# Kernel optimization log

Hardware: AMD Instinct MI355X
Metric: run time of the kernel (lower is better)

The kernel has to match this reference:

```python
import jax, jax.numpy as jnp
import numpy as np

N, CIN, C, COUT, K27, KNN_K = 65536, 1, 128, 128, 27, 16
C4, C2 = C // 4, C // 2


def _w(key, shape, fan_in):
    return (jax.random.normal(key, shape, dtype=jnp.float32) * (fan_in ** -0.5))


def setup_inputs() -> dict:
    key = jax.random.key(0)
    ks = jax.random.split(key, 32)
    inp = {
        "feats": jax.random.normal(ks[0], (N, CIN), dtype=jnp.float32),
        # kernel-map neighbor indices; value N means 'no neighbor at this offset'
        "nbr_idx": jax.random.randint(ks[1], (N, K27), 0, N + 1, dtype=jnp.int32),
        "knn_idx": jax.random.randint(ks[2], (N, KNN_K), 0, N, dtype=jnp.int32),
        "W_in": _w(ks[3], (K27, CIN, C), K27 * CIN), "b_in": jnp.zeros((C,), jnp.float32),
        "W_conv0": _w(ks[4], (3, K27, C, C), K27 * C), "b_conv0": jnp.zeros((3, C), jnp.float32),
        "W_conv1": _w(ks[5], (3, K27, C, C), K27 * C), "b_conv1": jnp.zeros((3, C), jnp.float32),
        "Wq": _w(ks[6], (3, C, C), C), "Wk": _w(ks[7], (3, C, C), C),
        "Wv": _w(ks[8], (3, C, C), C), "Wo": _w(ks[9], (3, C, C), C),
        "bo": jnp.zeros((3, C), jnp.float32),
        "W_a0": _w(ks[10], (3, C, C4), C), "b_a0": jnp.zeros((3, C4), jnp.float32),
        "W_a1": _w(ks[11], (3, K27, C4, C4), K27 * C4), "b_a1": jnp.zeros((3, C4), jnp.float32),
        "W_a2": _w(ks[12], (3, C4, C2), C4), "b_a2": jnp.zeros((3, C2), jnp.float32),
        "W_b0": _w(ks[13], (3, K27, C, C4), K27 * C), "b_b0": jnp.zeros((3, C4), jnp.float32),
        "W_b1": _w(ks[14], (3, K27, C4, C2), K27 * C4), "b_b1": jnp.zeros((3, C2), jnp.float32),
        "W_out": _w(ks[15], (K27, C, COUT), K27 * C), "b_out": jnp.zeros((COUT,), jnp.float32),
    }
    return inp


def sparse_conv(x, idx, W, b):
    # x: [N,Cin]; idx: [N,27] with pad value N -> zero feature
    xp = jnp.concatenate([x, jnp.zeros((1, x.shape[1]), x.dtype)], axis=0)
    g = xp[idx]  # [N,27,Cin]
    return jnp.einsum('nkc,kco->no', g, W) + b


def knn_attn(x, idx, Wq, Wk, Wv, Wo, bo):
    q = x @ Wq
    kf = x @ Wk
    vf = x @ Wv
    kn = kf[idx]  # [N,k,C]
    vn = vf[idx]
    logits = jnp.einsum('nc,nkc->nk', q, kn) * (x.shape[-1] ** -0.5)
    a = jax.nn.softmax(logits, axis=-1)
    agg = jnp.einsum('nk,nkc->nc', a, vn)
    return x + agg @ Wo + bo


def irn(x, idx, Wa0, ba0, Wa1, ba1, Wa2, ba2, Wb0, bb0, Wb1, bb1):
    r = jax.nn.relu
    h = r(x @ Wa0 + ba0)                      # 1x1 conv
    h = r(sparse_conv(h, idx, Wa1, ba1))       # 3x3x3
    out0 = r(h @ Wa2 + ba2)                    # 1x1 conv
    g = r(sparse_conv(x, idx, Wb0, bb0))
    out1 = r(sparse_conv(g, idx, Wb1, bb1))
    return jnp.concatenate([out0, out1], axis=-1) + x


def reference(feats, nbr_idx, knn_idx, W_in, b_in, W_conv0, b_conv0, W_conv1, b_conv1,
              Wq, Wk, Wv, Wo, bo, W_a0, b_a0, W_a1, b_a1, W_a2, b_a2,
              W_b0, b_b0, W_b1, b_b1, W_out, b_out):
    r = jax.nn.relu
    out = sparse_conv(feats, nbr_idx, W_in, b_in)
    for s in range(3):
        h = sparse_conv(out, nbr_idx, W_conv0[s], b_conv0[s])
        h = r(knn_attn(h, knn_idx, Wq[s], Wk[s], Wv[s], Wo[s], bo[s]))
        h = sparse_conv(h, nbr_idx, W_conv1[s], b_conv1[s])
        out = irn(h, nbr_idx, W_a0[s], b_a0[s], W_a1[s], b_a1[s], W_a2[s], b_a2[s],
                  W_b0[s], b_b0[s], W_b1[s], b_b1[s])
    return sparse_conv(out, nbr_idx, W_out, b_out)
```

## Files before the change

kernel.cpp:

```cpp
#include <hip/hip_runtime.h>
#include <stdint.h>

typedef unsigned short u16;
typedef __attribute__((ext_vector_type(8))) short bf16x8;
typedef __attribute__((ext_vector_type(4))) float f32x4;

#define NPTS 65536
#define NK27 27
#define KNN 16

__device__ __forceinline__ u16 f2b(float f) {
  union { float f; uint32_t u; } v; v.f = f;
  uint32_t r = (v.u + 0x7fffu + ((v.u >> 16) & 1u)) >> 16;
  return (u16)r;
}
__device__ __forceinline__ float b2f(u16 h) {
  union { uint32_t u; float f; } v; v.u = ((uint32_t)h) << 16; return v.f;
}

template<int N>
__device__ __forceinline__ void waitcnt_vm() {
  __builtin_amdgcn_s_waitcnt((N & 0xF) | ((N >> 4) << 14) | (0x7 << 4) | (0xF << 8));
}

__global__ __launch_bounds__(256) void wtrans(const float* __restrict__ src, u16* __restrict__ dst,
                                              int G, int CI, int CO) {
  int id = blockIdx.x * 256 + threadIdx.x;
  int tot = G * CI * CO;
  if (id >= tot) return;
  int cpr = CI / 8;
  int swzb = (cpr < 8 ? cpr : 8) - 1;
  int g = id / (CI * CO);
  int r = id - g * (CI * CO);
  int co = r / CI;
  int cis = r - co * CI;
  int c = cis / 8, e = cis - c * 8;
  int ci = (c ^ (co & swzb)) * 8 + e;
  dst[id] = f2b(src[(size_t)g * CI * CO + (size_t)ci * CO + co]);
}

__global__ __launch_bounds__(256) void wtrans_in(const float* __restrict__ W, u16* __restrict__ dst) {
  int id = blockIdx.x * 256 + threadIdx.x;
  if (id >= 128 * 32) return;
  int co = id >> 5, cis = id & 31;
  int c = cis >> 3, e = cis & 7;
  int ci = ((c ^ (co & 3)) << 3) | e;
  dst[id] = (ci < NK27) ? f2b(W[ci * 128 + co]) : (u16)0;
}

__global__ __launch_bounds__(256) void g27(const float* __restrict__ feats, const int* __restrict__ nbr,
                                           u16* __restrict__ G) {
  int id = blockIdx.x * 256 + threadIdx.x;
  int n = id >> 5, j = id & 31;
  u16 v = 0;
  if (j < NK27) {
    int m = nbr[n * NK27 + j];
    if (m < NPTS) v = f2b(feats[m]);
  }
  G[id] = v;
}

__global__ __launch_bounds__(256) void itrans(const int* __restrict__ nbr, int* __restrict__ out) {
  int id = blockIdx.x * 256 + threadIdx.x;
  int k = id >> 16;
  int n = id & (NPTS - 1);
  out[id] = nbr[n * NK27 + k];
}

__global__ void zero_pads(u16* a, u16* b, u16* c, u16* d, u16* e) {
  int t = threadIdx.x;
  if (t < 128) { a[t] = 0; b[t] = 0; c[t] = 0; }
  if (t < 32) { d[t] = 0; e[t] = 0; }
}

#define GLDS16(g, l)                                                                        \
  __builtin_amdgcn_global_load_lds((const __attribute__((address_space(1))) void*)(g),      \
                                   (__attribute__((address_space(3))) void*)(l), 16, 0, 0)

template<int CIN, int COUT, int NK, int EMODE, bool OUTF32>
__global__ __launch_bounds__(512, 2)
void sconv(const u16* __restrict__ x, const int* __restrict__ idxt,
           const u16* __restrict__ Wt, const float* __restrict__ bias,
           const u16* __restrict__ res, int res_stride,
           void* __restrict__ yout, int out_stride) {
  static_assert(NK == 1 || ((NK - 1) % 2 == 0), "NK odd or 1");
  constexpr int BM = 256;
  constexpr int KK = CIN / 32;
  constexpr int CPR = CIN / 8;
  constexpr int SWZB = (CPR < 8 ? CPR : 8) - 1;
  constexpr int N_REP = COUT / 16;
  constexpr int M_REP = 2;
  constexpr int BSZ = COUT * CIN;
  constexpr int BCH = BSZ / 8;
  constexpr int BISS = (BCH + 511) / 512;
  constexpr int AC = M_REP * KK;
  constexpr int IC = M_REP;
  constexpr int VC_F = AC + IC;
  constexpr int VC_L = AC;

  __shared__ __attribute__((aligned(16))) u16 Bs[2][BSZ];

  const int tid = threadIdx.x;
  const int lane = tid & 63;
  const int wave = tid >> 6;
  const int n0 = blockIdx.x * BM;
  const int lr = lane & 15;
  const int lh = lane >> 4;
  const int row0 = wave * 32;

  f32x4 acc[M_REP][N_REP];
#pragma unroll
  for (int i = 0; i < M_REP; ++i)
#pragma unroll
    for (int j = 0; j < N_REP; ++j) acc[i][j] = (f32x4){0.f, 0.f, 0.f, 0.f};

  bf16x8 A0[M_REP][KK], A1[M_REP][KK];
  int mna[M_REP], mnb[M_REP];

  auto stageB = [&](int k, u16* dst) {
    const u16* src = Wt + (size_t)k * BSZ;
#pragma unroll
    for (int i = 0; i < BISS; ++i) {
      int cb = i * 512 + wave * 64;
      if (BCH % 512 == 0 || cb < BCH)
        GLDS16(src + (size_t)(cb + lane) * 8, dst + (size_t)cb * 8);
    }
  };
  auto loadIdx = [&](int k, int (&m)[M_REP]) {
#pragma unroll
    for (int mr = 0; mr < M_REP; ++mr)
      m[mr] = idxt[(size_t)k * NPTS + n0 + row0 + mr * 16 + lr];
  };
  auto issueA = [&](const int (&m)[M_REP], bf16x8 (&dst)[M_REP][KK]) {
#pragma unroll
    for (int mr = 0; mr < M_REP; ++mr)
#pragma unroll
      for (int kk = 0; kk < KK; ++kk)
        dst[mr][kk] = *(const bf16x8*)(x + (size_t)m[mr] * CIN + kk * 32 + lh * 8);
  };
  auto compute = [&](const u16* bsp, const bf16x8 (&AR)[M_REP][KK]) {
#pragma unroll
    for (int kk = 0; kk < KK; ++kk) {
      bf16x8 b[N_REP];
      int pc = (kk * 4 + lh) ^ (lr & SWZB);
#pragma unroll
      for (int nr = 0; nr < N_REP; ++nr)
        b[nr] = *(const bf16x8*)(bsp + (size_t)(nr * 16 + lr) * CIN + pc * 8);
#pragma unroll
      for (int mr = 0; mr < M_REP; ++mr)
#pragma unroll
        for (int nr = 0; nr < N_REP; ++nr)
          acc[mr][nr] = __builtin_amdgcn_mfma_f32_16x16x32_bf16(AR[mr][kk], b[nr], acc[mr][nr], 0, 0, 0);
    }
  };

  if constexpr (NK == 1) {
    int m0[M_REP];
#pragma unroll
    for (int mr = 0; mr < M_REP; ++mr) m0[mr] = n0 + row0 + mr * 16 + lr;
    stageB(0, &Bs[0][0]);
    issueA(m0, A0);
    __syncthreads();
    compute(&Bs[0][0], A0);
  } else {
    int m0[M_REP];
    loadIdx(0, m0);
    __builtin_amdgcn_sched_barrier(0);
    stageB(0, &Bs[0][0]);
    __builtin_amdgcn_sched_barrier(0);
    issueA(m0, A0);
    __builtin_amdgcn_sched_barrier(0);
    loadIdx(1, mnb);
    __builtin_amdgcn_sched_barrier(0);

#define TAPX(kv, P, ACUR, ANXT, MUSE, MWRT)                                   \
    {                                                                         \
      const int k_ = (kv);                                                    \
      __builtin_amdgcn_sched_barrier(0);                                      \
      waitcnt_vm<VC_F>();                                                     \
      __builtin_amdgcn_s_barrier();                                           \
      __builtin_amdgcn_sched_barrier(0);                                      \
      stageB(k_ + 1, &Bs[(P) ^ 1][0]);                                        \
      __builtin_amdgcn_sched_barrier(0);                                      \
      issueA(MUSE, ANXT);                                                     \
      __builtin_amdgcn_sched_barrier(0);                                      \
      if (k_ + 2 < NK) loadIdx(k_ + 2, MWRT);                                 \
      __builtin_amdgcn_sched_barrier(0);                                      \
      compute(&Bs[P][0], ACUR);                                               \
    }

    for (int k = 0; k < NK - 1; k += 2) {
      TAPX(k, 0, A0, A1, mnb, mna);
      TAPX(k + 1, 1, A1, A0, mna, mnb);
    }
#undef TAPX
    __builtin_amdgcn_sched_barrier(0);
    waitcnt_vm<VC_L>();
    __builtin_amdgcn_s_barrier();
    __builtin_amdgcn_sched_barrier(0);
    compute(&Bs[0][0], A0);
  }

#pragma unroll
  for (int mr = 0; mr < M_REP; ++mr) {
#pragma unroll
    for (int nr = 0; nr < N_REP; ++nr) {
      int col = nr * 16 + lr;
      float bv = bias ? bias[col] : 0.0f;
#pragma unroll
      for (int j = 0; j < 4; ++j) {
        int n = n0 + row0 + mr * 16 + lh * 4 + j;
        float v = acc[mr][nr][j] + bv;
        if (EMODE == 1) v = fmaxf(v, 0.0f);
        else if (EMODE == 2) v = fmaxf(v + b2f(res[(size_t)n * res_stride + col]), 0.0f);
        else if (EMODE == 3) v = fmaxf(v, 0.0f) + b2f(res[(size_t)n * res_stride + col]);
        if (OUTF32) ((float*)yout)[(size_t)n * out_stride + col] = v;
        else ((u16*)yout)[(size_t)n * out_stride + col] = f2b(v);
      }
    }
  }
}

__global__ __launch_bounds__(256)
void attn_k(const u16* __restrict__ qb, const u16* __restrict__ kb,
            const u16* __restrict__ vb, const int* __restrict__ knn,
            u16* __restrict__ agg) {
  int n = (blockIdx.x * 256 + threadIdx.x) >> 6;
  int lane = threadIdx.x & 63;
  int c0 = lane * 2;
  uint32_t qp = *(const uint32_t*)(qb + (size_t)n * 128 + c0);
  float q0 = b2f((u16)(qp & 0xffff)), q1 = b2f((u16)(qp >> 16));
  float lg[KNN];
  int ms[KNN];
#pragma unroll
  for (int j = 0; j < KNN; ++j) {
    int m = knn[n * KNN + j];
    ms[j] = m;
    uint32_t kp = *(const uint32_t*)(kb + (size_t)m * 128 + c0);
    float p = q0 * b2f((u16)(kp & 0xffff)) + q1 * b2f((u16)(kp >> 16));
#pragma unroll
    for (int d = 1; d < 64; d <<= 1) p += __shfl_xor(p, d);
    lg[j] = p * 0.08838834764831845f;
  }
  float mx = lg[0];
#pragma unroll
  for (int j = 1; j < KNN; ++j) mx = fmaxf(mx, lg[j]);
  float s = 0.f, w[KNN];
#pragma unroll
  for (int j = 0; j < KNN; ++j) { w[j] = __expf(lg[j] - mx); s += w[j]; }
  float inv = 1.0f / s;
  float a0 = 0.f, a1 = 0.f;
#pragma unroll
  for (int j = 0; j < KNN; ++j) {
    uint32_t vp = *(const uint32_t*)(vb + (size_t)ms[j] * 128 + c0);
    a0 += w[j] * b2f((u16)(vp & 0xffff));
    a1 += w[j] * b2f((u16)(vp >> 16));
  }
  a0 *= inv; a1 *= inv;
  uint32_t op = (uint32_t)f2b(a0) | ((uint32_t)f2b(a1) << 16);
  *(uint32_t*)(agg + (size_t)n * 128 + c0) = op;
}

extern "C" void kernel_launch(void* const* d_in, const int* in_sizes, int n_in,
                              void* d_out, int out_size, void* d_ws, size_t ws_size,
                              hipStream_t stream) {
  (void)in_sizes; (void)n_in; (void)out_size; (void)ws_size;
  const float* feats = (const float*)d_in[0];
  const int*   nbr   = (const int*)d_in[1];
  const int*   knn   = (const int*)d_in[2];
  const float* W_in  = (const float*)d_in[3];
  const float* b_in  = (const float*)d_in[4];
  const float* W_c0  = (const float*)d_in[5];
  const float* b_c0  = (const float*)d_in[6];
  const float* W_c1  = (const float*)d_in[7];
  const float* b_c1  = (const float*)d_in[8];
  const float* Wq    = (const float*)d_in[9];
  const float* Wk    = (const float*)d_in[10];
  const float* Wv    = (const float*)d_in[11];
  const float* Wo    = (const float*)d_in[12];
  const float* bo    = (const float*)d_in[13];
  const float* Wa0   = (const float*)d_in[14];
  const float* ba0   = (const float*)d_in[15];
  const float* Wa1   = (const float*)d_in[16];
  const float* ba1   = (const float*)d_in[17];
  const float* Wa2   = (const float*)d_in[18];
  const float* ba2   = (const float*)d_in[19];
  const float* Wb0   = (const float*)d_in[20];
  const float* bb0   = (const float*)d_in[21];
  const float* Wb1   = (const float*)d_in[22];
  const float* bb1   = (const float*)d_in[23];
  const float* W_out = (const float*)d_in[24];
  const float* b_out = (const float*)d_in[25];

  char* ws = (char*)d_ws;
  size_t off = 0;
  auto alloc = [&](size_t bytes) { size_t r = off; off += (bytes + 255) & ~(size_t)255; return r; };

  u16* wt_c0  = (u16*)(ws + alloc((size_t)81 * 16384 * 2));
  u16* wt_c1  = (u16*)(ws + alloc((size_t)81 * 16384 * 2));
  u16* wt_q   = (u16*)(ws + alloc((size_t)3 * 16384 * 2));
  u16* wt_k   = (u16*)(ws + alloc((size_t)3 * 16384 * 2));
  u16* wt_v   = (u16*)(ws + alloc((size_t)3 * 16384 * 2));
  u16* wt_o   = (u16*)(ws + alloc((size_t)3 * 16384 * 2));
  u16* wt_a0  = (u16*)(ws + alloc((size_t)3 * 128 * 32 * 2));
  u16* wt_a1  = (u16*)(ws + alloc((size_t)81 * 32 * 32 * 2));
  u16* wt_a2  = (u16*)(ws + alloc((size_t)3 * 32 * 64 * 2));
  u16* wt_b0  = (u16*)(ws + alloc((size_t)81 * 128 * 32 * 2));
  u16* wt_b1  = (u16*)(ws + alloc((size_t)81 * 32 * 64 * 2));
  u16* wt_out = (u16*)(ws + alloc((size_t)27 * 16384 * 2));
  u16* wt_in  = (u16*)(ws + alloc((size_t)128 * 32 * 2));
  int* idx_t  = (int*)(ws + alloc((size_t)NK27 * NPTS * 4));
  u16* G27    = (u16*)(ws + alloc((size_t)NPTS * 32 * 2));

  u16* B0 = (u16*)(ws + alloc((size_t)(NPTS + 1) * 128 * 2));
  u16* B1 = (u16*)(ws + alloc((size_t)NPTS * 128 * 2));
  u16* KB = (u16*)(ws + alloc((size_t)(NPTS + 1) * 128 * 2));
  u16* VB = (u16*)(ws + alloc((size_t)(NPTS + 1) * 128 * 2));
  u16* QB = (u16*)(ws + alloc((size_t)NPTS * 128 * 2));
  u16* H1 = (u16*)(ws + alloc((size_t)(NPTS + 1) * 32 * 2));
  u16* HA = (u16*)(ws + alloc((size_t)NPTS * 32 * 2));
  u16* G  = (u16*)(ws + alloc((size_t)(NPTS + 1) * 32 * 2));
  u16* AGG = B0;
  u16* B2 = KB;
  u16* B3 = VB;

  auto TG = [](int tot) { return (tot + 255) / 256; };
  wtrans<<<TG(81 * 16384), 256, 0, stream>>>(W_c0, wt_c0, 81, 128, 128);
  wtrans<<<TG(81 * 16384), 256, 0, stream>>>(W_c1, wt_c1, 81, 128, 128);
  wtrans<<<TG(3 * 16384), 256, 0, stream>>>(Wq, wt_q, 3, 128, 128);
  wtrans<<<TG(3 * 16384), 256, 0, stream>>>(Wk, wt_k, 3, 128, 128);
  wtrans<<<TG(3 * 16384), 256, 0, stream>>>(Wv, wt_v, 3, 128, 128);
  wtrans<<<TG(3 * 16384), 256, 0, stream>>>(Wo, wt_o, 3, 128, 128);
  wtrans<<<TG(3 * 128 * 32), 256, 0, stream>>>(Wa0, wt_a0, 3, 128, 32);
  wtrans<<<TG(81 * 32 * 32), 256, 0, stream>>>(Wa1, wt_a1, 81, 32, 32);
  wtrans<<<TG(3 * 32 * 64), 256, 0, stream>>>(Wa2, wt_a2, 3, 32, 64);
  wtrans<<<TG(81 * 128 * 32), 256, 0, stream>>>(Wb0, wt_b0, 81, 128, 32);
  wtrans<<<TG(81 * 32 * 64), 256, 0, stream>>>(Wb1, wt_b1, 81, 32, 64);
  wtrans<<<TG(27 * 16384), 256, 0, stream>>>(W_out, wt_out, 27, 128, 128);
  wtrans_in<<<TG(128 * 32), 256, 0, stream>>>(W_in, wt_in);
  itrans<<<NK27 * NPTS / 256, 256, 0, stream>>>(nbr, idx_t);

  zero_pads<<<1, 256, 0, stream>>>(B0 + (size_t)NPTS * 128, KB + (size_t)NPTS * 128,
                                   VB + (size_t)NPTS * 128, H1 + (size_t)NPTS * 32,
                                   G + (size_t)NPTS * 32);

  g27<<<NPTS * 32 / 256, 256, 0, stream>>>(feats, nbr, G27);
  sconv<32, 128, 1, 0, false><<<NPTS / 256, 512, 0, stream>>>(G27, nullptr, wt_in, b_in, nullptr, 0, B0, 128);

  const int GB = NPTS / 256;
  for (int s = 0; s < 3; ++s) {
    const u16* wc0 = wt_c0 + (size_t)s * 27 * 16384;
    const u16* wc1 = wt_c1 + (size_t)s * 27 * 16384;
    const u16* wqs = wt_q + (size_t)s * 16384;
    const u16* wks = wt_k + (size_t)s * 16384;
    const u16* wvs = wt_v + (size_t)s * 16384;
    const u16* wos = wt_o + (size_t)s * 16384;
    const u16* wa0 = wt_a0 + (size_t)s * 4096;
    const u16* wa1 = wt_a1 + (size_t)s * 27648;
    const u16* wa2 = wt_a2 + (size_t)s * 2048;
    const u16* wb0 = wt_b0 + (size_t)s * 110592;
    const u16* wb1 = wt_b1 + (size_t)s * 55296;

    sconv<128, 128, 27, 0, false><<<GB, 512, 0, stream>>>(B0, idx_t, wc0, b_c0 + s * 128, nullptr, 0, B1, 128);
    sconv<128, 128, 1, 0, false><<<GB, 512, 0, stream>>>(B1, nullptr, wqs, nullptr, nullptr, 0, QB, 128);
    sconv<128, 128, 1, 0, false><<<GB, 512, 0, stream>>>(B1, nullptr, wks, nullptr, nullptr, 0, KB, 128);
    sconv<128, 128, 1, 0, false><<<GB, 512, 0, stream>>>(B1, nullptr, wvs, nullptr, nullptr, 0, VB, 128);
    attn_k<<<NPTS / 4, 256, 0, stream>>>(QB, KB, VB, knn, AGG);
    sconv<128, 128, 1, 2, false><<<GB, 512, 0, stream>>>(AGG, nullptr, wos, bo + s * 128, B1, 128, B2, 128);
    sconv<128, 128, 27, 0, false><<<GB, 512, 0, stream>>>(B2, idx_t, wc1, b_c1 + s * 128, nullptr, 0, B3, 128);
    sconv<128, 32, 1, 1, false><<<GB, 512, 0, stream>>>(B3, nullptr, wa0, ba0 + s * 32, nullptr, 0, H1, 32);
    sconv<32, 32, 27, 1, false><<<GB, 512, 0, stream>>>(H1, idx_t, wa1, ba1 + s * 32, nullptr, 0, HA, 32);
    sconv<32, 64, 1, 3, false><<<GB, 512, 0, stream>>>(HA, idx_t, wa2, ba2 + s * 64, B3, 128, B0, 128);
    sconv<128, 32, 27, 1, false><<<GB, 512, 0, stream>>>(B3, idx_t, wb0, bb0 + s * 32, nullptr, 0, G, 32);
    sconv<32, 64, 27, 3, false><<<GB, 512, 0, stream>>>(G, idx_t, wb1, bb1 + s * 64, B3 + 64, 128, (void*)(B0 + 64), 128);
  }
  sconv<128, 128, 27, 0, true><<<GB, 512, 0, stream>>>(B0, idx_t, wt_out, b_out, nullptr, 0, d_out, 128);
}
```

Before: 1.223 ms.

## Fuse Q/K/V projections into one kernel and widen attention per-lane work

Adds a qkv_k kernel that loads each block's activation tile once into registers and runs the three 128x128 projections back to back, reloading only the weight tile into shared memory. This replaces three separate GEMM launches that each re-read B1. The attention kernel is restructured so 16 lanes handle one point, each lane covering 8 channels with 16-byte loads. A 4-step shuffle reduction replaces the 6-step one, and the neighbour indices are fetched once and broadcast by shuffle. Register pressure in the fused kernel and the extra syncs between weight reloads are the tradeoff.

New measurement: 1.204 ms. About the same (-1.5%).

```diff
diff --git a/kernel.cpp b/kernel.cpp
--- a/kernel.cpp
+++ b/kernel.cpp
@@ -221,44 +221,144 @@
   }
 }
 
+__global__ __launch_bounds__(512, 2)
+void qkv_k(const u16* __restrict__ x, const u16* __restrict__ Wt,
+           u16* __restrict__ qo, u16* __restrict__ ko, u16* __restrict__ vo) {
+  constexpr int CIN = 128, COUT = 128;
+  constexpr int KK = 4, SWZB = 7, N_REP = 8, M_REP = 2;
+  constexpr int BSZ = COUT * CIN;
+  constexpr int BISS = (BSZ / 8) / 512;
+
+  __shared__ __attribute__((aligned(16))) u16 Bs[BSZ];
+
+  const int tid = threadIdx.x;
+  const int lane = tid & 63;
+  const int wave = tid >> 6;
+  const int n0 = blockIdx.x * 256;
+  const int lr = lane & 15;
+  const int lh = lane >> 4;
+  const int row0 = wave * 32;
+
+  bf16x8 A0[M_REP][KK];
+#pragma unroll
+  for (int mr = 0; mr < M_REP; ++mr)
+#pragma unroll
+    for (int kk = 0; kk < KK; ++kk)
+      A0[mr][kk] = *(const bf16x8*)(x + (size_t)(n0 + row0 + mr * 16 + lr) * CIN + kk * 32 + lh * 8);
+
+  u16* outs[3] = {qo, ko, vo};
+  for (int w = 0; w < 3; ++w) {
+    if (w) __syncthreads();
+    const u16* src = Wt + (size_t)w * BSZ;
+#pragma unroll
+    for (int i = 0; i < BISS; ++i) {
+      int cb = i * 512 + wave * 64;
+      GLDS16(src + (size_t)(cb + lane) * 8, &Bs[(size_t)cb * 8]);
+    }
+    __syncthreads();
+
+    f32x4 acc[M_REP][N_REP];
+#pragma unroll
+    for (int i = 0; i < M_REP; ++i)
+#pragma unroll
+      for (int j = 0; j < N_REP; ++j) acc[i][j] = (f32x4){0.f, 0.f, 0.f, 0.f};
+#pragma unroll
+    for (int kk = 0; kk < KK; ++kk) {
+      bf16x8 b[N_REP];
+      int pc = (kk * 4 + lh) ^ (lr & SWZB);
+#pragma unroll
+      for (int nr = 0; nr < N_REP; ++nr)
+        b[nr] = *(const bf16x8*)(&Bs[(size_t)(nr * 16 + lr) * CIN + pc * 8]);
+#pragma unroll
+      for (int mr = 0; mr < M_REP; ++mr)
+#pragma unroll
+        for (int nr = 0; nr < N_REP; ++nr)
+          acc[mr][nr] = __builtin_amdgcn_mfma_f32_16x16x32_bf16(A0[mr][kk], b[nr], acc[mr][nr], 0, 0, 0);
+    }
+    u16* yo = outs[w];
+#pragma unroll
+    for (int mr = 0; mr < M_REP; ++mr)
+#pragma unroll
+      for (int nr = 0; nr < N_REP; ++nr) {
+        int col = nr * 16 + lr;
+#pragma unroll
+        for (int j = 0; j < 4; ++j) {
+          int n = n0 + row0 + mr * 16 + lh * 4 + j;
+          yo[(size_t)n * 128 + col] = f2b(acc[mr][nr][j]);
+        }
+      }
+  }
+}
+
 __global__ __launch_bounds__(256)
 void attn_k(const u16* __restrict__ qb, const u16* __restrict__ kb,
             const u16* __restrict__ vb, const int* __restrict__ knn,
             u16* __restrict__ agg) {
-  int n = (blockIdx.x * 256 + threadIdx.x) >> 6;
-  int lane = threadIdx.x & 63;
-  int c0 = lane * 2;
-  uint32_t qp = *(const uint32_t*)(qb + (size_t)n * 128 + c0);
-  float q0 = b2f((u16)(qp & 0xffff)), q1 = b2f((u16)(qp >> 16));
+  const int t = blockIdx.x * 256 + threadIdx.x;
+  const int n = t >> 4;
+  const int s = t & 15;
+  const int lane = threadIdx.x & 63;
+  const int gbase = lane & 48;
+
+  int myidx = knn[n * KNN + s];
+
+  bf16x8 q8 = *(const bf16x8*)(qb + (size_t)n * 128 + s * 8);
+  float qf[8];
+#pragma unroll
+  for (int c = 0; c < 4; ++c) {
+    uint32_t u = ((const uint32_t*)&q8)[c];
+    qf[2 * c] = b2f((u16)(u & 0xffff));
+    qf[2 * c + 1] = b2f((u16)(u >> 16));
+  }
+
   float lg[KNN];
   int ms[KNN];
 #pragma unroll
   for (int j = 0; j < KNN; ++j) {
-    int m = knn[n * KNN + j];
-    ms[j] = m;
-    uint32_t kp = *(const uint32_t*)(kb + (size_t)m * 128 + c0);
-    float p = q0 * b2f((u16)(kp & 0xffff)) + q1 * b2f((u16)(kp >> 16));
-#pragma unroll
-    for (int d = 1; d < 64; d <<= 1) p += __shfl_xor(p, d);
-    lg[j] = p * 0.08838834764831845f;
+    int mj = __shfl(myidx, gbase | j);
+    ms[j] = mj;
+    bf16x8 k8 = *(const bf16x8*)(kb + (size_t)mj * 128 + s * 8);
+    float d = 0.f;
+#pragma unroll
+    for (int c = 0; c < 4; ++c) {
+      uint32_t u = ((const uint32_t*)&k8)[c];
+      d += qf[2 * c] * b2f((u16)(u & 0xffff));
+      d += qf[2 * c + 1] * b2f((u16)(u >> 16));
+    }
+    d += __shfl_xor(d, 1);
+    d += __shfl_xor(d, 2);
+    d += __shfl_xor(d, 4);
+    d += __shfl_xor(d, 8);
+    lg[j] = d * 0.08838834764831845f;
   }
   float mx = lg[0];
 #pragma unroll
   for (int j = 1; j < KNN; ++j) mx = fmaxf(mx, lg[j]);
-  float s = 0.f, w[KNN];
-#pragma unroll
-  for (int j = 0; j < KNN; ++j) { w[j] = __expf(lg[j] - mx); s += w[j]; }
-  float inv = 1.0f / s;
-  float a0 = 0.f, a1 = 0.f;
+  float ssum = 0.f;
+#pragma unroll
+  for (int j = 0; j < KNN; ++j) { lg[j] = __expf(lg[j] - mx); ssum += lg[j]; }
+  float inv = 1.0f / ssum;
+
+  float a[8] = {0, 0, 0, 0, 0, 0, 0, 0};
 #pragma unroll
   for (int j = 0; j < KNN; ++j) {
-    uint32_t vp = *(const uint32_t*)(vb + (size_t)ms[j] * 128 + c0);
-    a0 += w[j] * b2f((u16)(vp & 0xffff));
-    a1 += w[j] * b2f((u16)(vp >> 16));
-  }
-  a0 *= inv; a1 *= inv;
-  uint32_t op = (uint32_t)f2b(a0) | ((uint32_t)f2b(a1) << 16);
-  *(uint32_t*)(agg + (size_t)n * 128 + c0) = op;
+    bf16x8 v8 = *(const bf16x8*)(vb + (size_t)ms[j] * 128 + s * 8);
+    float w = lg[j];
+#pragma unroll
+    for (int c = 0; c < 4; ++c) {
+      uint32_t u = ((const uint32_t*)&v8)[c];
+      a[2 * c] += w * b2f((u16)(u & 0xffff));
+      a[2 * c + 1] += w * b2f((u16)(u >> 16));
+    }
+  }
+  uint32_t ow[4];
+#pragma unroll
+  for (int c = 0; c < 4; ++c)
+    ow[c] = (uint32_t)f2b(a[2 * c] * inv) | ((uint32_t)f2b(a[2 * c + 1] * inv) << 16);
+  *(uint32_t*)(agg + (size_t)n * 128 + s * 8 + 0) = ow[0];
+  *(uint32_t*)(agg + (size_t)n * 128 + s * 8 + 2) = ow[1];
+  *(uint32_t*)(agg + (size_t)n * 128 + s * 8 + 4) = ow[2];
+  *(uint32_t*)(agg + (size_t)n * 128 + s * 8 + 6) = ow[3];
 }
 
 extern "C" void kernel_launch(void* const* d_in, const int* in_sizes, int n_in,
@@ -298,9 +398,7 @@
 
   u16* wt_c0  = (u16*)(ws + alloc((size_t)81 * 16384 * 2));
   u16* wt_c1  = (u16*)(ws + alloc((size_t)81 * 16384 * 2));
-  u16* wt_q   = (u16*)(ws + alloc((size_t)3 * 16384 * 2));
-  u16* wt_k   = (u16*)(ws + alloc((size_t)3 * 16384 * 2));
-  u16* wt_v   = (u16*)(ws + alloc((size_t)3 * 16384 * 2));
+  u16* wt_qkv = (u16*)(ws + alloc((size_t)9 * 16384 * 2));
   u16* wt_o   = (u16*)(ws + alloc((size_t)3 * 16384 * 2));
   u16* wt_a0  = (u16*)(ws + alloc((size_t)3 * 128 * 32 * 2));
   u16* wt_a1  = (u16*)(ws + alloc((size_t)81 * 32 * 32 * 2));
@@ -327,9 +425,15 @@
   auto TG = [](int tot) { return (tot + 255) / 256; };
   wtrans<<<TG(81 * 16384), 256, 0, stream>>>(W_c0, wt_c0, 81, 128, 128);
   wtrans<<<TG(81 * 16384), 256, 0, stream>>>(W_c1, wt_c1, 81, 128, 128);
-  wtrans<<<TG(3 * 16384), 256, 0, stream>>>(Wq, wt_q, 3, 128, 128);
-  wtrans<<<TG(3 * 16384), 256, 0, stream>>>(Wk, wt_k, 3, 128, 128);
-  wtrans<<<TG(3 * 16384), 256, 0, stream>>>(Wv, wt_v, 3, 128, 128);
+  wtrans<<<TG(16384), 256, 0, stream>>>(Wq + 0 * 16384, wt_qkv + (size_t)0 * 16384, 1, 128, 128);
+  wtrans<<<TG(16384), 256, 0, stream>>>(Wk + 0 * 16384, wt_qkv + (size_t)1 * 16384, 1, 128, 128);
+  wtrans<<<TG(16384), 256, 0, stream>>>(Wv + 0 * 16384, wt_qkv + (size_t)2 * 16384, 1, 128, 128);
+  wtrans<<<TG(16384), 256, 0, stream>>>(Wq + 1 * 16384, wt_qkv + (size_t)3 * 16384, 1, 128, 128);
+  wtrans<<<TG(16384), 256, 0, stream>>>(Wk + 1 * 16384, wt_qkv + (size_t)4 * 16384, 1, 128, 128);
+  wtrans<<<TG(16384), 256, 0, stream>>>(Wv + 1 * 16384, wt_qkv + (size_t)5 * 16384, 1, 128, 128);
+  wtrans<<<TG(16384), 256, 0, stream>>>(Wq + 2 * 16384, wt_qkv + (size_t)6 * 16384, 1, 128, 128);
+  wtrans<<<TG(16384), 256, 0, stream>>>(Wk + 2 * 16384, wt_qkv + (size_t)7 * 16384, 1, 128, 128);
+  wtrans<<<TG(16384), 256, 0, stream>>>(Wv + 2 * 16384, wt_qkv + (size_t)8 * 16384, 1, 128, 128);
   wtrans<<<TG(3 * 16384), 256, 0, stream>>>(Wo, wt_o, 3, 128, 128);
   wtrans<<<TG(3 * 128 * 32), 256, 0, stream>>>(Wa0, wt_a0, 3, 128, 32);
   wtrans<<<TG(81 * 32 * 32), 256, 0, stream>>>(Wa1, wt_a1, 81, 32, 32);
@@ -351,9 +455,7 @@
   for (int s = 0; s < 3; ++s) {
     const u16* wc0 = wt_c0 + (size_t)s * 27 * 16384;
     const u16* wc1 = wt_c1 + (size_t)s * 27 * 16384;
-    const u16* wqs = wt_q + (size_t)s * 16384;
-    const u16* wks = wt_k + (size_t)s * 16384;
-    const u16* wvs = wt_v + (size_t)s * 16384;
+    const u16* wqkv = wt_qkv + (size_t)s * 3 * 16384;
     const u16* wos = wt_o + (size_t)s * 16384;
     const u16* wa0 = wt_a0 + (size_t)s * 4096;
     const u16* wa1 = wt_a1 + (size_t)s * 27648;
@@ -362,10 +464,8 @@
     const u16* wb1 = wt_b1 + (size_t)s * 55296;
 
     sconv<128, 128, 27, 0, false><<<GB, 512, 0, stream>>>(B0, idx_t, wc0, b_c0 + s * 128, nullptr, 0, B1, 128);
-    sconv<128, 128, 1, 0, false><<<GB, 512, 0, stream>>>(B1, nullptr, wqs, nullptr, nullptr, 0, QB, 128);
-    sconv<128, 128, 1, 0, false><<<GB, 512, 0, stream>>>(B1, nullptr, wks, nullptr, nullptr, 0, KB, 128);
-    sconv<128, 128, 1, 0, false><<<GB, 512, 0, stream>>>(B1, nullptr, wvs, nullptr, nullptr, 0, VB, 128);
-    attn_k<<<NPTS / 4, 256, 0, stream>>>(QB, KB, VB, knn, AGG);
+    qkv_k<<<GB, 512, 0, stream>>>(B1, wqkv, QB, KB, VB);
+    attn_k<<<NPTS / 16, 256, 0, stream>>>(QB, KB, VB, knn, AGG);
     sconv<128, 128, 1, 2, false><<<GB, 512, 0, stream>>>(AGG, nullptr, wos, bo + s * 128, B1, 128, B2, 128);
     sconv<128, 128, 27, 0, false><<<GB, 512, 0, stream>>>(B2, idx_t, wc1, b_c1 + s * 128, nullptr, 0, B3, 128);
     sconv<128, 32, 1, 1, false><<<GB, 512, 0, stream>>>(B3, nullptr, wa0, ba0 + s * 32, nullptr, 0, H1, 32);
```
